# Kernel optimization log

Hardware: AMD Instinct MI355X
Metric: run time of the kernel (lower is better)

The kernel has to match this reference:

```python
import jax, jax.numpy as jnp
import numpy as np

TEMP = 0.07
MOMENTUM = 0.2
K = 8192          # number of sampled negatives per row
NUM_CLASSES = 1000
B, N, D = 256, 32768, 2048
NEG_INF = -1e30


def _gumbel(key, shape):
    u = jax.random.uniform(key, shape, minval=1e-6, maxval=1.0)
    return -jnp.log(-jnp.log(u))


def setup_inputs() -> dict:
    key = jax.random.key(0)
    k1, k2, k3, k4, k5 = jax.random.split(key, 5)
    f = jax.random.normal(k1, (B, D), dtype=jnp.float32)
    f_nv = jax.random.normal(k2, (B, D), dtype=jnp.float32)
    # warmed-up memory bank (the real module L2-normalizes rows on update)
    features = jax.random.normal(k3, (N, D), dtype=jnp.float32)
    features = features / jnp.linalg.norm(features, axis=1, keepdims=True)
    labels = jax.random.randint(k4, (N,), 0, NUM_CLASSES)
    indexes = jax.random.randint(k5, (B,), 0, N)
    return {"f": f, "f_nv": f_nv, "features": features,
            "labels": labels, "indexes": indexes}


def reference(f, f_nv, features, labels, indexes):
    rkey = jax.random.key(42)
    kg1, kg2, kg3 = jax.random.split(rkey, 3)
    k = features                                   # [N, D] memory bank snapshot
    bsz = f.shape[0]

    # l_pos = <f_nv_i, k[indexes_i]>
    l_pos = jnp.sum(f_nv * k[indexes], axis=1, keepdims=True)   # [B, 1]

    mat = jnp.matmul(f, k.T)                       # [B, N]
    mat_sim = jnp.matmul(f_nv, k.T)                # [B, N]

    batch_labels = labels[indexes]                 # [B]
    pos_mask = labels[None, :] == batch_labels[:, None]         # [B, N]

    # torch.randperm-based sampling -> vectorized masked Gumbel sampling.
    # argmax of gumbel restricted to mask = uniform draw from masked set;
    # top-K of gumbel restricted to complement = K draws w/o replacement.
    g1 = _gumbel(kg1, (bsz, k.shape[0]))
    g2 = _gumbel(kg2, (bsz, k.shape[0]))
    g3 = _gumbel(kg3, (bsz, k.shape[0]))

    pos_idx_wogan = jnp.argmax(jnp.where(pos_mask, g1, NEG_INF), axis=1)
    positives_wogan = jnp.take_along_axis(mat, pos_idx_wogan[:, None], axis=1)  # [B,1]

    pos_idx = jnp.argmax(jnp.where(pos_mask, g2, NEG_INF), axis=1)
    positives = jnp.take_along_axis(mat_sim, pos_idx[:, None], axis=1)          # [B,1]

    _, neg_idx = jax.lax.top_k(jnp.where(pos_mask, NEG_INF, g3), K)             # [B,K]
    negatives = jnp.take_along_axis(mat_sim, neg_idx, axis=1)                   # [B,K]

    def ce_target0(logits):
        # CrossEntropyLoss with all targets == 0
        return -jax.nn.log_softmax(logits, axis=1)[:, 0].mean()

    self_out = jnp.concatenate([l_pos, negatives], axis=1) / TEMP
    inter_out = jnp.concatenate([positives, negatives], axis=1) / TEMP
    inter_out_wogan = jnp.concatenate([positives_wogan, negatives], axis=1) / TEMP

    memory_loss = ce_target0(self_out) + ce_target0(inter_out) + ce_target0(inter_out_wogan)

    # no-grad momentum update of the bank (F.normalize uses eps=1e-12)
    upd = MOMENTUM * k[indexes] + (1.0 - MOMENTUM) * f
    upd = upd / jnp.maximum(jnp.linalg.norm(upd, axis=1, keepdims=True), 1e-12)
    new_features = jax.lax.stop_gradient(features.at[indexes].set(upd))

    return memory_loss, new_features
```

## Files before the change

### kernel.cpp

```cpp
#include <hip/hip_runtime.h>
#include <stdint.h>

#define TEMP      0.07f
#define BATCH     256
#define NROWS     32768
#define DIM       2048
#define KNEG      8192
#define HALF_CNT  (BATCH * NROWS / 2)

#define RNG_MODE 0

typedef __attribute__((ext_vector_type(8))) short bf16x8;
typedef __attribute__((ext_vector_type(4))) float f32x4;

__host__ __device__ inline void tf2x32(uint32_t ka, uint32_t kb,
                                       uint32_t x0, uint32_t x1,
                                       uint32_t& o0, uint32_t& o1) {
  uint32_t ks2 = ka ^ kb ^ 0x1BD11BDAu;
#define TFR(r) { x0 += x1; x1 = (x1 << r) | (x1 >> (32 - r)); x1 ^= x0; }
  x0 += ka; x1 += kb;
  TFR(13) TFR(15) TFR(26) TFR(6)
  x0 += kb;  x1 += ks2 + 1u;
  TFR(17) TFR(29) TFR(16) TFR(24)
  x0 += ks2; x1 += ka + 2u;
  TFR(13) TFR(15) TFR(26) TFR(6)
  x0 += ka;  x1 += kb + 3u;
  TFR(17) TFR(29) TFR(16) TFR(24)
  x0 += kb;  x1 += ks2 + 4u;
  TFR(13) TFR(15) TFR(26) TFR(6)
  x0 += ks2; x1 += ka + 5u;
#undef TFR
  o0 = x0; o1 = x1;
}

__device__ inline uint32_t ubits_at(uint32_t ka, uint32_t kb, uint32_t q) {
#if RNG_MODE == 0
  uint32_t a, b; tf2x32(ka, kb, 0u, q, a, b);
  return (a ^ b) >> 9;
#else
  bool lo = q < HALF_CNT;
  uint32_t x0 = lo ? q : q - HALF_CNT;
  uint32_t x1 = lo ? q + HALF_CNT : q;
  uint32_t a, b; tf2x32(ka, kb, x0, x1, a, b);
  return (lo ? a : b) >> 9;
#endif
}

__device__ inline float block_sum(float v, float* sm) {
  __syncthreads();
  const int lane = threadIdx.x & 63;
  const int w = threadIdx.x >> 6;
  const int nw = blockDim.x >> 6;
  for (int o = 32; o; o >>= 1) v += __shfl_down(v, o, 64);
  if (lane == 0) sm[w] = v;
  __syncthreads();
  if (w == 0) {
    float x = (lane < nw) ? sm[lane] : 0.f;
    for (int o = 8; o; o >>= 1) x += __shfl_down(x, o, 64);
    if (lane == 0) sm[0] = x;
  }
  __syncthreads();
  return sm[0];
}

#define BM 128
#define BN 128
#define BKK 64

__device__ inline uint32_t pk2(float a, float b) {
  uint32_t ua = __float_as_uint(a), ub = __float_as_uint(b);
  ua = (ua + 0x7FFFu + ((ua >> 16) & 1u)) >> 16;
  ub = (ub + 0x7FFFu + ((ub >> 16) & 1u)) >> 16;
  return ua | (ub << 16);
}

__global__ __launch_bounds__(256) void gemm_matsim(
    const float* __restrict__ A,
    const float* __restrict__ B,
    float* __restrict__ C) {
  __shared__ short As[BM * BKK];
  __shared__ short Bs[BN * BKK];
  const int t = threadIdx.x;
  const int bm = blockIdx.x & 1;
  const int bn = blockIdx.x >> 1;
  const int row_a0 = bm * BM, row_b0 = bn * BN;
  const int lane = t & 63, wave = t >> 6;
  const int wr = wave >> 1, wc = wave & 1;
  const int srow = t >> 4, sc4 = t & 15;

  f32x4 acc[4][4] = {};

  for (int k0 = 0; k0 < DIM; k0 += BKK) {
    __syncthreads();
#pragma unroll
    for (int s = 0; s < 8; ++s) {
      int r = srow + 16 * s;
      const float4 va = *(const float4*)&A[(size_t)(row_a0 + r) * DIM + k0 + sc4 * 4];
      const float4 vb = *(const float4*)&B[(size_t)(row_b0 + r) * DIM + k0 + sc4 * 4];
      uint32_t off = (uint32_t)r * (BKK * 2) + (((uint32_t)sc4 * 8) ^ (((uint32_t)r & 7u) << 4));
      *(uint2*)((char*)As + off) = make_uint2(pk2(va.x, va.y), pk2(va.z, va.w));
      *(uint2*)((char*)Bs + off) = make_uint2(pk2(vb.x, vb.y), pk2(vb.z, vb.w));
    }
    __syncthreads();
#pragma unroll
    for (int kk = 0; kk < 2; ++kk) {
      bf16x8 af[4], bfr[4];
      const uint32_t kb = (uint32_t)(kk * 64 + ((lane >> 4) << 4));
#pragma unroll
      for (int m = 0; m < 4; ++m) {
        uint32_t rr = (uint32_t)(wr * 64 + m * 16 + (lane & 15));
        af[m] = *(const bf16x8*)((const char*)As + rr * (BKK * 2) + (kb ^ ((rr & 7u) << 4)));
      }
#pragma unroll
      for (int n = 0; n < 4; ++n) {
        uint32_t rr = (uint32_t)(wc * 64 + n * 16 + (lane & 15));
        bfr[n] = *(const bf16x8*)((const char*)Bs + rr * (BKK * 2) + (kb ^ ((rr & 7u) << 4)));
      }
#pragma unroll
      for (int m = 0; m < 4; ++m)
#pragma unroll
        for (int n = 0; n < 4; ++n)
          acc[m][n] = __builtin_amdgcn_mfma_f32_16x16x32_bf16(af[m], bfr[n], acc[m][n], 0, 0, 0);
    }
  }
  const int col_l = lane & 15, rg = (lane >> 4) * 4;
#pragma unroll
  for (int m = 0; m < 4; ++m)
#pragma unroll
    for (int n = 0; n < 4; ++n) {
      size_t base = (size_t)(row_a0 + wr * 64 + m * 16 + rg) * NROWS
                  + (size_t)(row_b0 + wc * 64 + n * 16 + col_l);
#pragma unroll
      for (int r = 0; r < 4; ++r)
        C[base + (size_t)r * NROWS] = acc[m][n][r];
    }
}

__global__ __launch_bounds__(1024) void sample_loss(
    const float* __restrict__ f, const float* __restrict__ f_nv,
    const float* __restrict__ features, const int* __restrict__ labels,
    const int* __restrict__ indexes, const float* __restrict__ mat_sim,
    float* __restrict__ row_loss,
    uint32_t k1a, uint32_t k1b, uint32_t k2a, uint32_t k2b,
    uint32_t k3a, uint32_t k3b) {
  __shared__ uint32_t keys[NROWS];
  __shared__ uint32_t hist[256];
  __shared__ unsigned long long am1, am2;
  __shared__ int tie_j[128];
  __shared__ int tie_cnt;
  __shared__ float sred[16];
  __shared__ float swm[16], sws[16];
  __shared__ uint32_t bc_prefix, bc_rem;
  __shared__ int blab_s;

  const int t = threadIdx.x;
  const int i = blockIdx.x;
  const size_t mbase = (size_t)i * NROWS;

  if (t == 0) {
    blab_s = labels[indexes[i]];
    am1 = 0ull; am2 = 0ull; tie_cnt = 0;
  }
  __syncthreads();
  const int blab = blab_s;

#pragma unroll 2
  for (int s = 0; s < NROWS / 1024; ++s) {
    int j = t + 1024 * s;
    uint32_t q = (uint32_t)i * NROWS + (uint32_t)j;
    int lab = labels[j];
    if (lab == blab) {
      keys[j] = 0u;
      unsigned long long lo = (unsigned long long)(uint32_t)(NROWS - 1 - j);
      uint32_t u1 = ubits_at(k1a, k1b, q);
      uint32_t u2 = ubits_at(k2a, k2b, q);
      atomicMax(&am1, ((unsigned long long)u1 << 32) | lo);
      atomicMax(&am2, ((unsigned long long)u2 << 32) | lo);
    } else {
      keys[j] = ubits_at(k3a, k3b, q);
    }
  }
  __syncthreads();

  const int jw = NROWS - 1 - (int)(unsigned)(am1 & 0xFFFFFFFFull);
  const int jp = NROWS - 1 - (int)(unsigned)(am2 & 0xFFFFFFFFull);

  const int bank = indexes[i];
  float d1 = 0.f, d2 = 0.f, d3 = 0.f;
  for (int d = t; d < DIM; d += 1024) {
    float fnv = f_nv[(size_t)i * DIM + d];
    d1 += fnv * features[(size_t)bank * DIM + d];
    d2 += f[(size_t)i * DIM + d] * features[(size_t)jw * DIM + d];
    d3 += fnv * features[(size_t)jp * DIM + d];
  }
  const float l_pos = block_sum(d1, sred);
  const float posw  = block_sum(d2, sred);
  const float posv  = block_sum(d3, sred);

  uint32_t prefix = 0, remaining = KNEG;
  const int shifts[3] = {15, 7, 0};
  const int nbits[3]  = {8, 8, 7};
  for (int p = 0; p < 3; ++p) {
    const int sh = shifts[p];
    const int nb = 1 << nbits[p];
    if (t < nb) hist[t] = 0u;
    __syncthreads();
    for (int s = 0; s < NROWS / 1024; ++s) {
      int j = t + 1024 * s;
      uint32_t k = keys[j];
      bool ok = (p == 0) || ((k >> (sh + nbits[p])) == prefix);
      if (ok) atomicAdd(&hist[(k >> sh) & (uint32_t)(nb - 1)], 1u);
    }
    __syncthreads();
    if (t == 0) {
      uint32_t c = 0; int b = nb - 1;
      for (;; --b) {
        c += hist[b];
        if (c >= remaining || b == 0) break;
      }
      bc_prefix = (prefix << nbits[p]) | (uint32_t)b;
      bc_rem = remaining - (c - hist[b]);
    }
    __syncthreads();
    prefix = bc_prefix; remaining = bc_rem;
  }
  const uint32_t T = prefix;
  const uint32_t need = remaining;

  float m = -INFINITY, ssum = 0.f;
  for (int s = 0; s < NROWS / 1024; ++s) {
    int j = t + 1024 * s;
    uint32_t k = keys[j];
    if (k > T) {
      float v = mat_sim[mbase + j] / TEMP;
      if (v <= m) ssum += expf(v - m);
      else { ssum = ssum * expf(m - v) + 1.0f; m = v; }
    } else if (k == T) {
      int p = atomicAdd(&tie_cnt, 1);
      if (p < 128) tie_j[p] = j;
    }
  }
  for (int o = 32; o; o >>= 1) {
    float m2 = __shfl_down(m, o, 64);
    float s2 = __shfl_down(ssum, o, 64);
    if (m2 > m) { ssum = ssum * expf(m - m2) + s2; m = m2; }
    else if (m2 != -INFINITY) ssum += s2 * expf(m2 - m);
  }
  if ((t & 63) == 0) { swm[t >> 6] = m; sws[t >> 6] = ssum; }
  __syncthreads();
  if (t < 64) {
    float mm = (t < 16) ? swm[t] : -INFINITY;
    float ss = (t < 16) ? sws[t] : 0.f;
    for (int o = 8; o; o >>= 1) {
      float m2 = __shfl_down(mm, o, 64);
      float s2 = __shfl_down(ss, o, 64);
      if (m2 > mm) { ss = ss * expf(mm - m2) + s2; mm = m2; }
      else if (m2 != -INFINITY) ss += s2 * expf(m2 - mm);
    }
    if (t == 0) { swm[0] = mm; sws[0] = ss; }
  }
  __syncthreads();

  if (t == 0) {
    float M = swm[0], S = sws[0];
    int tc = tie_cnt;
    if (tc <= 128) {
      for (int a2 = 1; a2 < tc; ++a2) {
        int v = tie_j[a2]; int b2 = a2 - 1;
        while (b2 >= 0 && tie_j[b2] > v) { tie_j[b2 + 1] = tie_j[b2]; --b2; }
        tie_j[b2 + 1] = v;
      }
      for (uint32_t r = 0; r < need; ++r) {
        float v = mat_sim[mbase + tie_j[r]] / TEMP;
        if (v <= M) S += expf(v - M);
        else { S = S * expf(M - v) + 1.0f; M = v; }
      }
    } else {
      uint32_t taken = 0;
      for (int j = 0; j < NROWS && taken < need; ++j) {
        if (keys[j] == T) {
          float v = mat_sim[mbase + j] / TEMP;
          if (v <= M) S += expf(v - M);
          else { S = S * expf(M - v) + 1.0f; M = v; }
          ++taken;
        }
      }
    }
    float lp = l_pos / TEMP, pv = posv / TEMP, pw = posw / TEMP;
    float L = 0.f;
    { float X = fmaxf(M, lp); L += X + logf(expf(lp - X) + S * expf(M - X)) - lp; }
    { float X = fmaxf(M, pv); L += X + logf(expf(pv - X) + S * expf(M - X)) - pv; }
    { float X = fmaxf(M, pw); L += X + logf(expf(pw - X) + S * expf(M - X)) - pw; }
    row_loss[i] = L;
  }
}

__global__ void finalize_loss(const float* __restrict__ row_loss,
                              float* __restrict__ out) {
  __shared__ float sm[4];
  int t = threadIdx.x;
  float v = row_loss[t];
  for (int o = 32; o; o >>= 1) v += __shfl_down(v, o, 64);
  if ((t & 63) == 0) sm[t >> 6] = v;
  __syncthreads();
  if (t == 0) out[0] = (sm[0] + sm[1] + sm[2] + sm[3]) * (1.0f / BATCH);
}

__global__ void copy_features(const float* __restrict__ src,
                              float* __restrict__ dst) {
  const int n = NROWS * DIM;
  const int stride = gridDim.x * blockDim.x;
  int idx = blockIdx.x * blockDim.x + threadIdx.x;
  for (; idx + 3 * stride < n; idx += 4 * stride) {
    float a0 = src[idx];
    float a1 = src[idx + stride];
    float a2 = src[idx + 2 * stride];
    float a3 = src[idx + 3 * stride];
    dst[idx] = a0; dst[idx + stride] = a1;
    dst[idx + 2 * stride] = a2; dst[idx + 3 * stride] = a3;
  }
  for (; idx < n; idx += stride) dst[idx] = src[idx];
}

__global__ __launch_bounds__(256) void update_rows(
    const float* __restrict__ f, const float* __restrict__ features,
    const int* __restrict__ indexes, float* __restrict__ outF) {
  __shared__ float sred[16];
  const int i = blockIdx.x;
  const int row = indexes[i];
  for (int i2 = i + 1; i2 < BATCH; ++i2)
    if (indexes[i2] == row) return;
  const int t = threadIdx.x;
  float ss = 0.f;
  for (int d = t; d < DIM; d += 256) {
    float u = 0.2f * features[(size_t)row * DIM + d] + 0.8f * f[(size_t)i * DIM + d];
    ss += u * u;
  }
  ss = block_sum(ss, sred);
  float nrm = fmaxf(sqrtf(ss), 1e-12f);
  for (int d = t; d < DIM; d += 256) {
    float u = 0.2f * features[(size_t)row * DIM + d] + 0.8f * f[(size_t)i * DIM + d];
    outF[(size_t)row * DIM + d] = u / nrm;
  }
}

extern "C" void kernel_launch(void* const* d_in, const int* in_sizes, int n_in,
                              void* d_out, int out_size, void* d_ws, size_t ws_size,
                              hipStream_t stream) {
  (void)in_sizes; (void)n_in; (void)out_size; (void)d_ws; (void)ws_size;
  const float* f        = (const float*)d_in[0];
  const float* f_nv     = (const float*)d_in[1];
  const float* features = (const float*)d_in[2];
  const int*   labels   = (const int*)d_in[3];
  const int*   indexes  = (const int*)d_in[4];
  float* out = (float*)d_out;

  float* mat_sim  = out + 4;
  float* row_loss = out + 4 + (size_t)BATCH * NROWS;

  uint32_t c[6];
#if RNG_MODE == 0
  { uint32_t a, b;
    tf2x32(0u, 42u, 0u, 0u, a, b); c[0] = a; c[1] = b;
    tf2x32(0u, 42u, 0u, 1u, a, b); c[2] = a; c[3] = b;
    tf2x32(0u, 42u, 0u, 2u, a, b); c[4] = a; c[5] = b; }
#else
  { uint32_t a, b;
    tf2x32(0u, 42u, 0u, 3u, a, b); c[0] = a; c[3] = b;
    tf2x32(0u, 42u, 1u, 4u, a, b); c[1] = a; c[4] = b;
    tf2x32(0u, 42u, 2u, 5u, a, b); c[2] = a; c[5] = b; }
#endif

  gemm_matsim<<<dim3(512), dim3(256), 0, stream>>>(f_nv, features, mat_sim);
  sample_loss<<<dim3(BATCH), dim3(1024), 0, stream>>>(
      f, f_nv, features, labels, indexes, mat_sim, row_loss,
      c[0], c[1], c[2], c[3], c[4], c[5]);
  finalize_loss<<<dim3(1), dim3(256), 0, stream>>>(row_loss, out);
  copy_features<<<dim3(4096), dim3(256), 0, stream>>>(features, out + 1);
  update_rows<<<dim3(BATCH), dim3(256), 0, stream>>>(f, features, indexes, out + 1);
}
```

Baseline: 345.1 us.

## Fuse feature-bank copy into double-buffered GEMM, widen tiles, split histograms

After: 289.0 us. 16.3% less time.

```diff
diff --git a/kernel.cpp b/kernel.cpp
--- a/kernel.cpp
+++ b/kernel.cpp
@@ -6,9 +6,6 @@
 #define NROWS     32768
 #define DIM       2048
 #define KNEG      8192
-#define HALF_CNT  (BATCH * NROWS / 2)
-
-#define RNG_MODE 0
 
 typedef __attribute__((ext_vector_type(8))) short bf16x8;
 typedef __attribute__((ext_vector_type(4))) float f32x4;
@@ -34,16 +31,8 @@
 }
 
 __device__ inline uint32_t ubits_at(uint32_t ka, uint32_t kb, uint32_t q) {
-#if RNG_MODE == 0
   uint32_t a, b; tf2x32(ka, kb, 0u, q, a, b);
   return (a ^ b) >> 9;
-#else
-  bool lo = q < HALF_CNT;
-  uint32_t x0 = lo ? q : q - HALF_CNT;
-  uint32_t x1 = lo ? q + HALF_CNT : q;
-  uint32_t a, b; tf2x32(ka, kb, x0, x1, a, b);
-  return (lo ? a : b) >> 9;
-#endif
 }
 
 __device__ inline float block_sum(float v, float* sm) {
@@ -63,9 +52,10 @@
   return sm[0];
 }
 
-#define BM 128
+#define BM 256
 #define BN 128
-#define BKK 64
+#define BK 64
+#define NT (DIM / BK)
 
 __device__ inline uint32_t pk2(float a, float b) {
   uint32_t ua = __float_as_uint(a), ub = __float_as_uint(b);
@@ -74,66 +64,112 @@
   return ua | (ub << 16);
 }
 
-__global__ __launch_bounds__(256) void gemm_matsim(
+__global__ __launch_bounds__(512, 2) void gemm_fused(
     const float* __restrict__ A,
     const float* __restrict__ B,
-    float* __restrict__ C) {
-  __shared__ short As[BM * BKK];
-  __shared__ short Bs[BN * BKK];
+    float* __restrict__ C,
+    float* __restrict__ outF,
+    int copy_skip_rows) {
+  __shared__ short As[2][BM * BK];
+  __shared__ short Bs[2][BN * BK];
   const int t = threadIdx.x;
-  const int bm = blockIdx.x & 1;
-  const int bn = blockIdx.x >> 1;
-  const int row_a0 = bm * BM, row_b0 = bn * BN;
+  const int bn = blockIdx.x;
   const int lane = t & 63, wave = t >> 6;
-  const int wr = wave >> 1, wc = wave & 1;
-  const int srow = t >> 4, sc4 = t & 15;
-
-  f32x4 acc[4][4] = {};
-
-  for (int k0 = 0; k0 < DIM; k0 += BKK) {
-    __syncthreads();
-#pragma unroll
-    for (int s = 0; s < 8; ++s) {
-      int r = srow + 16 * s;
-      const float4 va = *(const float4*)&A[(size_t)(row_a0 + r) * DIM + k0 + sc4 * 4];
-      const float4 vb = *(const float4*)&B[(size_t)(row_b0 + r) * DIM + k0 + sc4 * 4];
-      uint32_t off = (uint32_t)r * (BKK * 2) + (((uint32_t)sc4 * 8) ^ (((uint32_t)r & 7u) << 4));
-      *(uint2*)((char*)As + off) = make_uint2(pk2(va.x, va.y), pk2(va.z, va.w));
-      *(uint2*)((char*)Bs + off) = make_uint2(pk2(vb.x, vb.y), pk2(vb.z, vb.w));
-    }
-    __syncthreads();
-#pragma unroll
-    for (int kk = 0; kk < 2; ++kk) {
-      bf16x8 af[4], bfr[4];
-      const uint32_t kb = (uint32_t)(kk * 64 + ((lane >> 4) << 4));
-#pragma unroll
-      for (int m = 0; m < 4; ++m) {
-        uint32_t rr = (uint32_t)(wr * 64 + m * 16 + (lane & 15));
-        af[m] = *(const bf16x8*)((const char*)As + rr * (BKK * 2) + (kb ^ ((rr & 7u) << 4)));
-      }
-#pragma unroll
-      for (int n = 0; n < 4; ++n) {
-        uint32_t rr = (uint32_t)(wc * 64 + n * 16 + (lane & 15));
-        bfr[n] = *(const bf16x8*)((const char*)Bs + rr * (BKK * 2) + (kb ^ ((rr & 7u) << 4)));
-      }
-#pragma unroll
-      for (int m = 0; m < 4; ++m)
-#pragma unroll
-        for (int n = 0; n < 4; ++n)
-          acc[m][n] = __builtin_amdgcn_mfma_f32_16x16x32_bf16(af[m], bfr[n], acc[m][n], 0, 0, 0);
-    }
-  }
+  const int wr = wave >> 2, wc = wave & 3;
+  const int ld_row = t >> 4;
+  const int ld_c4 = t & 15;
+
+  float4 ra[8], rb[4];
+  f32x4 acc[8][2] = {};
+
+#define LOADT(k0)                                                              \
+  {                                                                            \
+    _Pragma("unroll")                                                          \
+    for (int s = 0; s < 8; ++s)                                                \
+      ra[s] = *(const float4*)&A[(size_t)(ld_row + 32 * s) * DIM + (k0) + ld_c4 * 4]; \
+    _Pragma("unroll")                                                          \
+    for (int s = 0; s < 4; ++s)                                                \
+      rb[s] = *(const float4*)&B[(size_t)(bn * BN + ld_row + 32 * s) * DIM + (k0) + ld_c4 * 4]; \
+  }
+
+#define WRITET(buf, k0)                                                        \
+  {                                                                            \
+    _Pragma("unroll")                                                          \
+    for (int s = 0; s < 8; ++s) {                                              \
+      int r = ld_row + 32 * s;                                                 \
+      uint32_t off = (uint32_t)r * (BK * 2) +                                  \
+                     (((uint32_t)ld_c4 * 8) ^ (((uint32_t)r & 7u) << 4));      \
+      *(uint2*)((char*)As[buf] + off) =                                        \
+          make_uint2(pk2(ra[s].x, ra[s].y), pk2(ra[s].z, ra[s].w));            \
+    }                                                                          \
+    _Pragma("unroll")                                                          \
+    for (int s = 0; s < 4; ++s) {                                              \
+      int r = ld_row + 32 * s;                                                 \
+      uint32_t off = (uint32_t)r * (BK * 2) +                                  \
+                     (((uint32_t)ld_c4 * 8) ^ (((uint32_t)r & 7u) << 4));      \
+      *(uint2*)((char*)Bs[buf] + off) =                                        \
+          make_uint2(pk2(rb[s].x, rb[s].y), pk2(rb[s].z, rb[s].w));            \
+      int g = bn * BN + r;                                                     \
+      if (g >= copy_skip_rows) {                                               \
+        float* d = &outF[(size_t)g * DIM + (k0) + ld_c4 * 4];                  \
+        d[0] = rb[s].x; d[1] = rb[s].y; d[2] = rb[s].z; d[3] = rb[s].w;        \
+      }                                                                        \
+    }                                                                          \
+  }
+
+#define COMPUTET(buf)                                                          \
+  {                                                                            \
+    _Pragma("unroll")                                                          \
+    for (int kk = 0; kk < 2; ++kk) {                                           \
+      bf16x8 af[8], bfr[2];                                                    \
+      const uint32_t kb = (uint32_t)(kk * 64 + ((lane >> 4) << 4));            \
+      _Pragma("unroll")                                                        \
+      for (int m = 0; m < 8; ++m) {                                            \
+        uint32_t rr = (uint32_t)(wr * 128 + m * 16 + (lane & 15));             \
+        af[m] = *(const bf16x8*)((const char*)As[buf] + rr * (BK * 2) +        \
+                                 (kb ^ ((rr & 7u) << 4)));                     \
+      }                                                                        \
+      _Pragma("unroll")                                                        \
+      for (int n = 0; n < 2; ++n) {                                            \
+        uint32_t rr = (uint32_t)(wc * 32 + n * 16 + (lane & 15));              \
+        bfr[n] = *(const bf16x8*)((const char*)Bs[buf] + rr * (BK * 2) +       \
+                                  (kb ^ ((rr & 7u) << 4)));                    \
+      }                                                                        \
+      _Pragma("unroll")                                                        \
+      for (int m = 0; m < 8; ++m)                                              \
+        _Pragma("unroll")                                                      \
+        for (int n = 0; n < 2; ++n)                                            \
+          acc[m][n] = __builtin_amdgcn_mfma_f32_16x16x32_bf16(                 \
+              af[m], bfr[n], acc[m][n], 0, 0, 0);                              \
+    }                                                                          \
+  }
+
+  LOADT(0);
+  WRITET(0, 0);
+  __syncthreads();
+  for (int t0 = 0; t0 < NT; ++t0) {
+    if (t0 + 1 < NT) LOADT((t0 + 1) * BK);
+    COMPUTET(t0 & 1);
+    if (t0 + 1 < NT) {
+      WRITET((t0 + 1) & 1, (t0 + 1) * BK);
+      __syncthreads();
+    }
+  }
+
   const int col_l = lane & 15, rg = (lane >> 4) * 4;
 #pragma unroll
-  for (int m = 0; m < 4; ++m)
+  for (int m = 0; m < 8; ++m)
 #pragma unroll
-    for (int n = 0; n < 4; ++n) {
-      size_t base = (size_t)(row_a0 + wr * 64 + m * 16 + rg) * NROWS
-                  + (size_t)(row_b0 + wc * 64 + n * 16 + col_l);
+    for (int n = 0; n < 2; ++n) {
+      size_t base = (size_t)(wr * 128 + m * 16 + rg) * NROWS
+                  + (size_t)(bn * BN + wc * 32 + n * 16 + col_l);
 #pragma unroll
       for (int r = 0; r < 4; ++r)
         C[base + (size_t)r * NROWS] = acc[m][n][r];
     }
+#undef LOADT
+#undef WRITET
+#undef COMPUTET
 }
 
 __global__ __launch_bounds__(1024) void sample_loss(
@@ -144,6 +180,7 @@
     uint32_t k1a, uint32_t k1b, uint32_t k2a, uint32_t k2b,
     uint32_t k3a, uint32_t k3b) {
   __shared__ uint32_t keys[NROWS];
+  __shared__ uint32_t hist4[4][256];
   __shared__ uint32_t hist[256];
   __shared__ unsigned long long am1, am2;
   __shared__ int tie_j[128];
@@ -203,14 +240,17 @@
   for (int p = 0; p < 3; ++p) {
     const int sh = shifts[p];
     const int nb = 1 << nbits[p];
-    if (t < nb) hist[t] = 0u;
+    ((uint32_t*)hist4)[t] = 0u;
     __syncthreads();
+    const int hsel = t >> 8;
     for (int s = 0; s < NROWS / 1024; ++s) {
       int j = t + 1024 * s;
       uint32_t k = keys[j];
       bool ok = (p == 0) || ((k >> (sh + nbits[p])) == prefix);
-      if (ok) atomicAdd(&hist[(k >> sh) & (uint32_t)(nb - 1)], 1u);
-    }
+      if (ok) atomicAdd(&hist4[hsel][(k >> sh) & (uint32_t)(nb - 1)], 1u);
+    }
+    __syncthreads();
+    if (t < nb) hist[t] = hist4[0][t] + hist4[1][t] + hist4[2][t] + hist4[3][t];
     __syncthreads();
     if (t == 0) {
       uint32_t c = 0; int b = nb - 1;
@@ -306,20 +346,15 @@
   if (t == 0) out[0] = (sm[0] + sm[1] + sm[2] + sm[3]) * (1.0f / BATCH);
 }
 
-__global__ void copy_features(const float* __restrict__ src,
-                              float* __restrict__ dst) {
-  const int n = NROWS * DIM;
-  const int stride = gridDim.x * blockDim.x;
+__global__ void copy_front(const float* __restrict__ src,
+                           float* __restrict__ dst, int n4) {
   int idx = blockIdx.x * blockDim.x + threadIdx.x;
-  for (; idx + 3 * stride < n; idx += 4 * stride) {
-    float a0 = src[idx];
-    float a1 = src[idx + stride];
-    float a2 = src[idx + 2 * stride];
-    float a3 = src[idx + 3 * stride];
-    dst[idx] = a0; dst[idx + stride] = a1;
-    dst[idx + 2 * stride] = a2; dst[idx + 3 * stride] = a3;
-  }
-  for (; idx < n; idx += stride) dst[idx] = src[idx];
+  int stride = gridDim.x * blockDim.x;
+  for (int i = idx; i < n4; i += stride) {
+    float4 v = *(const float4*)&src[(size_t)i * 4];
+    float* d = &dst[(size_t)i * 4];
+    d[0] = v.x; d[1] = v.y; d[2] = v.z; d[3] = v.w;
+  }
 }
 
 __global__ __launch_bounds__(256) void update_rows(
@@ -347,7 +382,7 @@
 extern "C" void kernel_launch(void* const* d_in, const int* in_sizes, int n_in,
                               void* d_out, int out_size, void* d_ws, size_t ws_size,
                               hipStream_t stream) {
-  (void)in_sizes; (void)n_in; (void)out_size; (void)d_ws; (void)ws_size;
+  (void)in_sizes; (void)n_in; (void)out_size;
   const float* f        = (const float*)d_in[0];
   const float* f_nv     = (const float*)d_in[1];
   const float* features = (const float*)d_in[2];
@@ -355,27 +390,36 @@
   const int*   indexes  = (const int*)d_in[4];
   float* out = (float*)d_out;
 
-  float* mat_sim  = out + 4;
-  float* row_loss = out + 4 + (size_t)BATCH * NROWS;
+  const size_t need = ((size_t)BATCH * NROWS + 256) * sizeof(float);
+  float* mat_sim;
+  float* row_loss;
+  int skip_rows;
+  bool use_ws = (d_ws != nullptr) && (ws_size >= need);
+  if (use_ws) {
+    mat_sim = (float*)d_ws;
+    row_loss = mat_sim + (size_t)BATCH * NROWS;
+    skip_rows = 0;
+  } else {
+    mat_sim = out + 4;
+    row_loss = out + 4 + (size_t)BATCH * NROWS;
+    skip_rows = 4224;
+  }
 
   uint32_t c[6];
-#if RNG_MODE == 0
   { uint32_t a, b;
     tf2x32(0u, 42u, 0u, 0u, a, b); c[0] = a; c[1] = b;
     tf2x32(0u, 42u, 0u, 1u, a, b); c[2] = a; c[3] = b;
     tf2x32(0u, 42u, 0u, 2u, a, b); c[4] = a; c[5] = b; }
-#else
-  { uint32_t a, b;
-    tf2x32(0u, 42u, 0u, 3u, a, b); c[0] = a; c[3] = b;
-    tf2x32(0u, 42u, 1u, 4u, a, b); c[1] = a; c[4] = b;
-    tf2x32(0u, 42u, 2u, 5u, a, b); c[2] = a; c[5] = b; }
-#endif
-
-  gemm_matsim<<<dim3(512), dim3(256), 0, stream>>>(f_nv, features, mat_sim);
+
+  gemm_fused<<<dim3(NROWS / BN), dim3(512), 0, stream>>>(
+      f_nv, features, mat_sim, out + 1, skip_rows);
   sample_loss<<<dim3(BATCH), dim3(1024), 0, stream>>>(
       f, f_nv, features, labels, indexes, mat_sim, row_loss,
       c[0], c[1], c[2], c[3], c[4], c[5]);
   finalize_loss<<<dim3(1), dim3(256), 0, stream>>>(row_loss, out);
-  copy_features<<<dim3(4096), dim3(256), 0, stream>>>(features, out + 1);
+  if (!use_ws) {
+    copy_front<<<dim3(2048), dim3(256), 0, stream>>>(
+        features, out + 1, 4224 * DIM / 4);
+  }
   update_rows<<<dim3(BATCH), dim3(256), 0, stream>>>(f, features, indexes, out + 1);
 }
```
